# Kernel optimization log

Measured on AMD Instinct MI355X. Metric: run time of the kernel, lower is better.

The kernel has to match this reference:

```python
import jax, jax.numpy as jnp
import numpy as np

LAYERS = 3
EMB = 256
B = 4096
N_ITEMS = 50000
MAX_LEN = 50
EPS = 1e-12  # F.normalize eps


def setup_inputs() -> dict:
    key = jax.random.key(0)
    k1, k2, k3, k4, k5, k6 = jax.random.split(key, 6)
    item_embedding = jax.random.normal(k1, (N_ITEMS, EMB), dtype=jnp.float32)
    D = jax.random.uniform(k2, (B, B), dtype=jnp.float32)
    A = jax.random.uniform(k3, (B, B), dtype=jnp.float32)
    # indices into padded table of size N_ITEMS+1 (row 0 is the zero pad row)
    session_item = jax.random.randint(k4, (B, MAX_LEN), 0, N_ITEMS + 1, dtype=jnp.int64)
    session_len = jax.random.randint(k5, (B, 1), 1, MAX_LEN + 1).astype(jnp.float32)
    w_sess = jax.random.normal(k6, (LAYERS, EMB, EMB), dtype=jnp.float32) * (1.0 / np.sqrt(EMB))
    return {"item_embedding": item_embedding, "D": D, "A": A,
            "session_item": session_item, "session_len": session_len,
            "w_sess": w_sess}


def reference(item_embedding, D, A, session_item, session_len, w_sess):
    # prepend zero pad row, then gather: [B, L, E]
    emb = jnp.concatenate([jnp.zeros((1, item_embedding.shape[1]), item_embedding.dtype),
                           item_embedding], axis=0)
    seq_h = emb[session_item]                      # fused gather (no host round-trip)
    session_emb = seq_h.sum(axis=1) / session_len  # [B, E] mean pooling

    DA = D @ A                                     # [B, B]
    acc = session_emb                              # layer-0 (unnormalized) term
    x = session_emb
    for i in range(LAYERS):
        x = x @ w_sess[i].T                        # torch Linear: y = x W^T
        x = DA @ x                                 # dense GCN propagation
        norm = jnp.maximum(jnp.linalg.norm(x, axis=-1, keepdims=True), EPS)
        acc = acc + x / norm                       # normalized copy stored; x stays raw
    return acc / (LAYERS + 1)
```

## Files before the change

kernel.cpp:

```cpp
#include <hip/hip_runtime.h>
#include <hip/hip_bf16.h>
#include <cstdint>
#include <cstddef>

#define LAYERS 3
#define EMB 256
#define NB 4096
#define MAXLEN 50
#define NITEMS 50000

typedef float f32x4 __attribute__((ext_vector_type(4)));
typedef __bf16 bf16x8 __attribute__((ext_vector_type(8)));
typedef unsigned short u16;

static __device__ __forceinline__ u16 f2bf(float f) {
  union { float f; uint32_t u; } v; v.f = f;
  uint32_t r = v.u + 0x7FFFu + ((v.u >> 16) & 1u);
  return (u16)(r >> 16);
}

static __device__ __forceinline__ float bf2f(u16 h) {
  union { uint32_t u; float f; } v; v.u = (uint32_t)h << 16; return v.f;
}

static __device__ __forceinline__ f32x4 bfu4(ushort4 h) {
  f32x4 r; r.x = bf2f(h.x); r.y = bf2f(h.y); r.z = bf2f(h.z); r.w = bf2f(h.w);
  return r;
}

static __device__ __forceinline__ ushort4 f2bf4(f32x4 v) {
  ushort4 o; o.x = f2bf(v.x); o.y = f2bf(v.y); o.z = f2bf(v.z); o.w = f2bf(v.w);
  return o;
}

template <typename T> __device__ __forceinline__ T cvt_out(float v);
template <> __device__ __forceinline__ float cvt_out<float>(float v) { return v; }
template <> __device__ __forceinline__ u16 cvt_out<u16>(float v) { return f2bf(v); }

#define N4_D (NB * NB / 4)
#define N4_W (LAYERS * EMB * EMB / 4)
#define N4_E ((NITEMS + 1) * EMB / 4)

__global__ void pack_all(const float* __restrict__ D, const float* __restrict__ A,
                         const float* __restrict__ w, const float* __restrict__ emb,
                         u16* __restrict__ Db, u16* __restrict__ Ab,
                         u16* __restrict__ wb, u16* __restrict__ ebp) {
  const int total = N4_D + N4_D + N4_W + N4_E;
  for (int i = blockIdx.x * blockDim.x + threadIdx.x; i < total;
       i += gridDim.x * blockDim.x) {
    int j = i;
    if (j < N4_D) {
      reinterpret_cast<ushort4*>(Db)[j] = f2bf4(reinterpret_cast<const f32x4*>(D)[j]);
    } else if ((j -= N4_D) < N4_D) {
      reinterpret_cast<ushort4*>(Ab)[j] = f2bf4(reinterpret_cast<const f32x4*>(A)[j]);
    } else if ((j -= N4_D) < N4_W) {
      reinterpret_cast<ushort4*>(wb)[j] = f2bf4(reinterpret_cast<const f32x4*>(w)[j]);
    } else {
      j -= N4_W;
      ushort4 o = {0, 0, 0, 0};
      if (j >= EMB / 4) o = f2bf4(reinterpret_cast<const f32x4*>(emb)[j - EMB / 4]);
      reinterpret_cast<ushort4*>(ebp)[j] = o;
    }
  }
}

__global__ void gather_mean(const u16* __restrict__ ebp, const int* __restrict__ items,
                            const float* __restrict__ slen, float* __restrict__ acc,
                            u16* __restrict__ xb) {
  int w = threadIdx.x >> 6, lane = threadIdx.x & 63;
  int b = blockIdx.x * 4 + w;
  f32x4 s = {0.f, 0.f, 0.f, 0.f};
  const int* it = items + (size_t)b * MAXLEN;
  const int le = lane * 4;
#pragma unroll 2
  for (int l = 0; l < MAXLEN; l += 5) {
    int i0 = it[l], i1 = it[l + 1], i2 = it[l + 2], i3 = it[l + 3], i4 = it[l + 4];
    ushort4 v0 = *reinterpret_cast<const ushort4*>(ebp + (size_t)i0 * EMB + le);
    ushort4 v1 = *reinterpret_cast<const ushort4*>(ebp + (size_t)i1 * EMB + le);
    ushort4 v2 = *reinterpret_cast<const ushort4*>(ebp + (size_t)i2 * EMB + le);
    ushort4 v3 = *reinterpret_cast<const ushort4*>(ebp + (size_t)i3 * EMB + le);
    ushort4 v4 = *reinterpret_cast<const ushort4*>(ebp + (size_t)i4 * EMB + le);
    s += bfu4(v0) + bfu4(v1) + bfu4(v2) + bfu4(v3) + bfu4(v4);
  }
  float inv = 1.0f / slen[b];
  s *= inv;
  *reinterpret_cast<f32x4*>(acc + (size_t)b * EMB + le) = s;
  *reinterpret_cast<ushort4*>(xb + (size_t)b * EMB + le) = f2bf4(s);
}

template <typename OUT_T>
__global__ __launch_bounds__(256, 3) void gemm_bt(const u16* __restrict__ Am,
                                                  const u16* __restrict__ Bt,
                                                  OUT_T* __restrict__ C,
                                                  int M, int N, int K, size_t zstride) {
  __shared__ __align__(16) u16 As[128 * 64];
  __shared__ __align__(16) u16 Bs[128 * 64];
  const int tid = threadIdx.x;
  const int lane = tid & 63;
  const int wid = tid >> 6;
  const int wr = wid >> 1, wc = wid & 1;
  const int row0 = blockIdx.y * 128, col0 = blockIdx.x * 128;
  const int kslice = K / (int)gridDim.z;
  const int kb = blockIdx.z * kslice, ke = kb + kslice;
  C += (size_t)blockIdx.z * zstride;

  f32x4 acc[4][4];
#pragma unroll
  for (int m = 0; m < 4; m++)
#pragma unroll
    for (int n = 0; n < 4; n++)
#pragma unroll
      for (int j = 0; j < 4; j++) acc[m][n][j] = 0.0f;

  const int lrow = lane & 15;
  const int lhi = lane >> 4;
  const int sw7 = lane & 7;
  const int cswz = ((lane & 7) ^ (lane >> 3)) * 8;
  const int srow = wid * 8 + (lane >> 3);

  for (int k0 = kb; k0 < ke; k0 += 64) {
#pragma unroll
    for (int i = 0; i < 4; i++) {
      int r = i * 32 + srow;
      __builtin_amdgcn_global_load_lds(
          (__attribute__((address_space(1))) void*)(Am + (size_t)(row0 + r) * K + k0 + cswz),
          (__attribute__((address_space(3))) void*)(As + (size_t)(i * 256 + wid * 64) * 8),
          16, 0, 0);
      __builtin_amdgcn_global_load_lds(
          (__attribute__((address_space(1))) void*)(Bt + (size_t)(col0 + r) * K + k0 + cswz),
          (__attribute__((address_space(3))) void*)(Bs + (size_t)(i * 256 + wid * 64) * 8),
          16, 0, 0);
    }
    __syncthreads();

#pragma unroll
    for (int kk = 0; kk < 2; kk++) {
      const int co = ((kk * 4 + lhi) ^ sw7) * 8;
      bf16x8 af[4], bfv[4];
#pragma unroll
      for (int m = 0; m < 4; m++)
        af[m] = *reinterpret_cast<const bf16x8*>(As + (wr * 64 + m * 16 + lrow) * 64 + co);
#pragma unroll
      for (int n = 0; n < 4; n++)
        bfv[n] = *reinterpret_cast<const bf16x8*>(Bs + (wc * 64 + n * 16 + lrow) * 64 + co);
#pragma unroll
      for (int m = 0; m < 4; m++)
#pragma unroll
        for (int n = 0; n < 4; n++)
          acc[m][n] = __builtin_amdgcn_mfma_f32_16x16x32_bf16(af[m], bfv[n], acc[m][n], 0, 0, 0);
    }
    __syncthreads();
  }

#pragma unroll
  for (int m = 0; m < 4; m++) {
#pragma unroll
    for (int j = 0; j < 4; j++) {
      int r = row0 + wr * 64 + m * 16 + lhi * 4 + j;
      OUT_T* cp = C + (size_t)r * N + col0 + wc * 64 + lrow;
#pragma unroll
      for (int n = 0; n < 4; n++) cp[n * 16] = cvt_out<OUT_T>(acc[m][n][j]);
    }
  }
}

__global__ __launch_bounds__(256) void gemm_bt64(const u16* __restrict__ Am,
                                                 const u16* __restrict__ Bt,
                                                 u16* __restrict__ C,
                                                 int M, int N, int K) {
  __shared__ u16 As[64 * 32];
  __shared__ u16 Bs[64 * 32];
  const int tid = threadIdx.x;
  const int lane = tid & 63;
  const int wid = tid >> 6;
  const int wr = wid >> 1, wc = wid & 1;
  const int row0 = blockIdx.y * 64, col0 = blockIdx.x * 64;

  f32x4 acc[2][2];
#pragma unroll
  for (int m = 0; m < 2; m++)
#pragma unroll
    for (int n = 0; n < 2; n++)
#pragma unroll
      for (int j = 0; j < 4; j++) acc[m][n][j] = 0.0f;

  const int lrow = lane & 15;
  const int lko = (lane >> 4) * 8;

  for (int k0 = 0; k0 < K; k0 += 32) {
    int r = tid >> 2, c = (tid & 3) * 8;
    const u16* gA = Am + (size_t)(row0 + r) * K + k0 + c;
    const u16* gB = Bt + (size_t)(col0 + r) * K + k0 + c;
    __builtin_amdgcn_global_load_lds(
        (__attribute__((address_space(1))) void*)gA,
        (__attribute__((address_space(3))) void*)(As + (size_t)(wid * 64) * 8), 16, 0, 0);
    __builtin_amdgcn_global_load_lds(
        (__attribute__((address_space(1))) void*)gB,
        (__attribute__((address_space(3))) void*)(Bs + (size_t)(wid * 64) * 8), 16, 0, 0);
    __syncthreads();

    bf16x8 af[2], bfv[2];
#pragma unroll
    for (int m = 0; m < 2; m++)
      af[m] = *reinterpret_cast<const bf16x8*>(As + (wr * 32 + m * 16 + lrow) * 32 + lko);
#pragma unroll
    for (int n = 0; n < 2; n++)
      bfv[n] = *reinterpret_cast<const bf16x8*>(Bs + (wc * 32 + n * 16 + lrow) * 32 + lko);
#pragma unroll
    for (int m = 0; m < 2; m++)
#pragma unroll
      for (int n = 0; n < 2; n++)
        acc[m][n] = __builtin_amdgcn_mfma_f32_16x16x32_bf16(af[m], bfv[n], acc[m][n], 0, 0, 0);
    __syncthreads();
  }

#pragma unroll
  for (int m = 0; m < 2; m++) {
#pragma unroll
    for (int j = 0; j < 4; j++) {
      int r = row0 + wr * 32 + m * 16 + (lane >> 4) * 4 + j;
      u16* cp = C + (size_t)r * N + col0 + wc * 32 + (lane & 15);
#pragma unroll
      for (int n = 0; n < 2; n++) cp[n * 16] = f2bf(acc[m][n][j]);
    }
  }
}

__global__ void uredux(const u16* __restrict__ zp, u16* __restrict__ uT,
                       int n4, int nsplit, size_t zstride4) {
  int i = blockIdx.x * blockDim.x + threadIdx.x;
  if (i < n4) {
    f32x4 s = {0.f, 0.f, 0.f, 0.f};
    for (int k = 0; k < nsplit; k++)
      s += bfu4(reinterpret_cast<const ushort4*>(zp)[(size_t)k * zstride4 + i]);
    reinterpret_cast<ushort4*>(uT)[i] = f2bf4(s);
  }
}

__global__ void norm_acc(const u16* __restrict__ zp, size_t zstride, int nsplit,
                         float* __restrict__ acc, u16* __restrict__ xb,
                         float* __restrict__ outp, int fin) {
  int b = blockIdx.x, t = threadIdx.x;
  size_t i = (size_t)b * EMB + t;
  float v = 0.0f;
  for (int s = 0; s < nsplit; s++) v += bf2f(zp[(size_t)s * zstride + i]);
  float s2 = v * v;
#pragma unroll
  for (int o = 32; o > 0; o >>= 1) s2 += __shfl_down(s2, o, 64);
  __shared__ float ws4[4];
  if ((t & 63) == 0) ws4[t >> 6] = s2;
  __syncthreads();
  float tot = ws4[0] + ws4[1] + ws4[2] + ws4[3];
  float rn = 1.0f / fmaxf(sqrtf(tot), 1e-12f);
  if (fin) {
    outp[i] = (acc[i] + v * rn) * 0.25f;
  } else {
    acc[i] += v * rn;
    xb[i] = f2bf(v);
  }
}

extern "C" void kernel_launch(void* const* d_in, const int* in_sizes, int n_in,
                              void* d_out, int out_size, void* d_ws, size_t ws_size,
                              hipStream_t stream) {
  const float* emb   = (const float*)d_in[0];
  const float* D     = (const float*)d_in[1];
  const float* A     = (const float*)d_in[2];
  const int*   items = (const int*)d_in[3];
  const float* slen  = (const float*)d_in[4];
  const float* w     = (const float*)d_in[5];
  float* out = (float*)d_out;

  char* p = (char*)d_ws;
  u16* Db   = (u16*)p;   p += (size_t)NB * NB * 2;
  u16* Ab   = (u16*)p;   p += (size_t)NB * NB * 2;
  float* accf = (float*)p; p += (size_t)NB * EMB * 4;
  u16* xb   = (u16*)p;   p += (size_t)NB * EMB * 2;
  u16* yT   = (u16*)p;   p += (size_t)EMB * NB * 2;
  u16* uT   = (u16*)p;   p += (size_t)EMB * NB * 2;
  u16* wb   = (u16*)p;   p += (size_t)LAYERS * EMB * EMB * 2;
  u16* ebp  = (u16*)p;   p += (size_t)(NITEMS + 1) * EMB * 2;
  u16* zp   = ebp;

  pack_all<<<2048, 256, 0, stream>>>(D, A, w, emb, Db, Ab, wb, ebp);
  gather_mean<<<NB / 4, 256, 0, stream>>>(ebp, items, slen, accf, xb);

  for (int i = 0; i < LAYERS; i++) {
    gemm_bt64<<<dim3(NB / 64, EMB / 64), 256, 0, stream>>>(wb + (size_t)i * EMB * EMB, xb, yT,
                                                           EMB, NB, EMB);
    gemm_bt<u16><<<dim3(NB / 128, EMB / 128, 8), 256, 0, stream>>>(
        yT, Ab, zp, EMB, NB, NB, (size_t)EMB * NB);
    uredux<<<EMB * NB / 4 / 256, 256, 0, stream>>>(zp, uT, EMB * NB / 4, 8,
                                                   (size_t)EMB * NB / 4);
    gemm_bt<u16><<<dim3(EMB / 128, NB / 128, 8), 256, 0, stream>>>(
        Db, uT, zp, NB, EMB, NB, (size_t)NB * EMB);
    norm_acc<<<NB, 256, 0, stream>>>(zp, (size_t)NB * EMB, 8, accf, xb, out, i == LAYERS - 1);
  }
}
```

Before: 214.1 us.

## Drop bf16 pre-packing and feed fp32 D/A/embeddings directly into kernels

Removes the up-front pack kernel that converted D, A and the whole embedding table to bf16. The big split-K GEMMs now stage fp32 tiles of D or A into LDS and convert them to bf16 while loading fragments. The gather reads fp32 embeddings with index-minus-one and masks the pad row. The small weight GEMM now loads its full K=256 tile in one pass instead of looping. The aim is to drop the conversion pass and its large write traffic, at the cost of reading fp32 D and A in every layer, doubling LDS tile size and adding conversion work inside the GEMM inner loop.

```diff
diff --git a/kernel.cpp b/kernel.cpp
--- a/kernel.cpp
+++ b/kernel.cpp
@@ -37,34 +37,12 @@
 template <> __device__ __forceinline__ float cvt_out<float>(float v) { return v; }
 template <> __device__ __forceinline__ u16 cvt_out<u16>(float v) { return f2bf(v); }
 
-#define N4_D (NB * NB / 4)
-#define N4_W (LAYERS * EMB * EMB / 4)
-#define N4_E ((NITEMS + 1) * EMB / 4)
-
-__global__ void pack_all(const float* __restrict__ D, const float* __restrict__ A,
-                         const float* __restrict__ w, const float* __restrict__ emb,
-                         u16* __restrict__ Db, u16* __restrict__ Ab,
-                         u16* __restrict__ wb, u16* __restrict__ ebp) {
-  const int total = N4_D + N4_D + N4_W + N4_E;
-  for (int i = blockIdx.x * blockDim.x + threadIdx.x; i < total;
-       i += gridDim.x * blockDim.x) {
-    int j = i;
-    if (j < N4_D) {
-      reinterpret_cast<ushort4*>(Db)[j] = f2bf4(reinterpret_cast<const f32x4*>(D)[j]);
-    } else if ((j -= N4_D) < N4_D) {
-      reinterpret_cast<ushort4*>(Ab)[j] = f2bf4(reinterpret_cast<const f32x4*>(A)[j]);
-    } else if ((j -= N4_D) < N4_W) {
-      reinterpret_cast<ushort4*>(wb)[j] = f2bf4(reinterpret_cast<const f32x4*>(w)[j]);
-    } else {
-      j -= N4_W;
-      ushort4 o = {0, 0, 0, 0};
-      if (j >= EMB / 4) o = f2bf4(reinterpret_cast<const f32x4*>(emb)[j - EMB / 4]);
-      reinterpret_cast<ushort4*>(ebp)[j] = o;
-    }
-  }
-}
-
-__global__ void gather_mean(const u16* __restrict__ ebp, const int* __restrict__ items,
+__global__ void pack_w(const float* __restrict__ in, u16* __restrict__ out) {
+  int i = blockIdx.x * blockDim.x + threadIdx.x;
+  reinterpret_cast<ushort4*>(out)[i] = f2bf4(reinterpret_cast<const f32x4*>(in)[i]);
+}
+
+__global__ void gather_mean(const float* __restrict__ emb, const int* __restrict__ items,
                             const float* __restrict__ slen, float* __restrict__ acc,
                             u16* __restrict__ xb) {
   int w = threadIdx.x >> 6, lane = threadIdx.x & 63;
@@ -75,12 +53,13 @@
 #pragma unroll 2
   for (int l = 0; l < MAXLEN; l += 5) {
     int i0 = it[l], i1 = it[l + 1], i2 = it[l + 2], i3 = it[l + 3], i4 = it[l + 4];
-    ushort4 v0 = *reinterpret_cast<const ushort4*>(ebp + (size_t)i0 * EMB + le);
-    ushort4 v1 = *reinterpret_cast<const ushort4*>(ebp + (size_t)i1 * EMB + le);
-    ushort4 v2 = *reinterpret_cast<const ushort4*>(ebp + (size_t)i2 * EMB + le);
-    ushort4 v3 = *reinterpret_cast<const ushort4*>(ebp + (size_t)i3 * EMB + le);
-    ushort4 v4 = *reinterpret_cast<const ushort4*>(ebp + (size_t)i4 * EMB + le);
-    s += bfu4(v0) + bfu4(v1) + bfu4(v2) + bfu4(v3) + bfu4(v4);
+    f32x4 v0 = *reinterpret_cast<const f32x4*>(emb + (size_t)(i0 > 0 ? i0 - 1 : 0) * EMB + le);
+    f32x4 v1 = *reinterpret_cast<const f32x4*>(emb + (size_t)(i1 > 0 ? i1 - 1 : 0) * EMB + le);
+    f32x4 v2 = *reinterpret_cast<const f32x4*>(emb + (size_t)(i2 > 0 ? i2 - 1 : 0) * EMB + le);
+    f32x4 v3 = *reinterpret_cast<const f32x4*>(emb + (size_t)(i3 > 0 ? i3 - 1 : 0) * EMB + le);
+    f32x4 v4 = *reinterpret_cast<const f32x4*>(emb + (size_t)(i4 > 0 ? i4 - 1 : 0) * EMB + le);
+    s += v0 * (i0 > 0 ? 1.f : 0.f) + v1 * (i1 > 0 ? 1.f : 0.f) + v2 * (i2 > 0 ? 1.f : 0.f) +
+         v3 * (i3 > 0 ? 1.f : 0.f) + v4 * (i4 > 0 ? 1.f : 0.f);
   }
   float inv = 1.0f / slen[b];
   s *= inv;
@@ -88,13 +67,54 @@
   *reinterpret_cast<ushort4*>(xb + (size_t)b * EMB + le) = f2bf4(s);
 }
 
-template <typename OUT_T>
-__global__ __launch_bounds__(256, 3) void gemm_bt(const u16* __restrict__ Am,
-                                                  const u16* __restrict__ Bt,
+template <bool F32>
+__device__ __forceinline__ void stage_tile(const void* __restrict__ g, char* lds, int rbase,
+                                           int K, int k0, int tid, int wid) {
+  constexpr int CPR = F32 ? 16 : 8;
+  constexpr int NLD = F32 ? 8 : 4;
+#pragma unroll
+  for (int i = 0; i < NLD; i++) {
+    int row = i * (256 / CPR) + (tid / CPR);
+    int sc = (tid % CPR) ^ (row & 7);
+    if constexpr (F32) {
+      const float* src = (const float*)g + (size_t)(rbase + row) * K + k0 + sc * 4;
+      __builtin_amdgcn_global_load_lds(
+          (const __attribute__((address_space(1))) void*)src,
+          (__attribute__((address_space(3))) void*)(lds + (i * 256 + wid * 64) * 16), 16, 0, 0);
+    } else {
+      const u16* src = (const u16*)g + (size_t)(rbase + row) * K + k0 + sc * 8;
+      __builtin_amdgcn_global_load_lds(
+          (const __attribute__((address_space(1))) void*)src,
+          (__attribute__((address_space(3))) void*)(lds + (i * 256 + wid * 64) * 16), 16, 0, 0);
+    }
+  }
+}
+
+template <bool F32>
+__device__ __forceinline__ bf16x8 ld_frag(const char* lds, int row_, int kk, int lhi, int sw7) {
+  if constexpr (F32) {
+    const float* p = (const float*)lds + (size_t)row_ * 64;
+    int cp = kk * 8 + lhi * 2;
+    f32x4 lo = *reinterpret_cast<const f32x4*>(p + ((cp ^ sw7) * 4));
+    f32x4 hi = *reinterpret_cast<const f32x4*>(p + (((cp + 1) ^ sw7) * 4));
+    bf16x8 r;
+    r[0] = (__bf16)lo[0]; r[1] = (__bf16)lo[1]; r[2] = (__bf16)lo[2]; r[3] = (__bf16)lo[3];
+    r[4] = (__bf16)hi[0]; r[5] = (__bf16)hi[1]; r[6] = (__bf16)hi[2]; r[7] = (__bf16)hi[3];
+    return r;
+  } else {
+    const u16* p = (const u16*)lds + (size_t)row_ * 64;
+    int co = ((kk * 4 + lhi) ^ sw7) * 8;
+    return *reinterpret_cast<const bf16x8*>(p + co);
+  }
+}
+
+template <bool AF32, bool BF32, typename OUT_T>
+__global__ __launch_bounds__(256, 3) void gemm_mx(const void* __restrict__ Av,
+                                                  const void* __restrict__ Bv,
                                                   OUT_T* __restrict__ C,
                                                   int M, int N, int K, size_t zstride) {
-  __shared__ __align__(16) u16 As[128 * 64];
-  __shared__ __align__(16) u16 Bs[128 * 64];
+  __shared__ __align__(16) char As[128 * 64 * (AF32 ? 4 : 2)];
+  __shared__ __align__(16) char Bs[128 * 64 * (BF32 ? 4 : 2)];
   const int tid = threadIdx.x;
   const int lane = tid & 63;
   const int wid = tid >> 6;
@@ -115,34 +135,21 @@
   const int lrow = lane & 15;
   const int lhi = lane >> 4;
   const int sw7 = lane & 7;
-  const int cswz = ((lane & 7) ^ (lane >> 3)) * 8;
-  const int srow = wid * 8 + (lane >> 3);
 
   for (int k0 = kb; k0 < ke; k0 += 64) {
-#pragma unroll
-    for (int i = 0; i < 4; i++) {
-      int r = i * 32 + srow;
-      __builtin_amdgcn_global_load_lds(
-          (__attribute__((address_space(1))) void*)(Am + (size_t)(row0 + r) * K + k0 + cswz),
-          (__attribute__((address_space(3))) void*)(As + (size_t)(i * 256 + wid * 64) * 8),
-          16, 0, 0);
-      __builtin_amdgcn_global_load_lds(
-          (__attribute__((address_space(1))) void*)(Bt + (size_t)(col0 + r) * K + k0 + cswz),
-          (__attribute__((address_space(3))) void*)(Bs + (size_t)(i * 256 + wid * 64) * 8),
-          16, 0, 0);
-    }
+    stage_tile<AF32>(Av, As, row0, K, k0, tid, wid);
+    stage_tile<BF32>(Bv, Bs, col0, K, k0, tid, wid);
     __syncthreads();
 
 #pragma unroll
     for (int kk = 0; kk < 2; kk++) {
-      const int co = ((kk * 4 + lhi) ^ sw7) * 8;
       bf16x8 af[4], bfv[4];
 #pragma unroll
       for (int m = 0; m < 4; m++)
-        af[m] = *reinterpret_cast<const bf16x8*>(As + (wr * 64 + m * 16 + lrow) * 64 + co);
+        af[m] = ld_frag<AF32>(As, wr * 64 + m * 16 + lrow, kk, lhi, sw7);
 #pragma unroll
       for (int n = 0; n < 4; n++)
-        bfv[n] = *reinterpret_cast<const bf16x8*>(Bs + (wc * 64 + n * 16 + lrow) * 64 + co);
+        bfv[n] = ld_frag<BF32>(Bs, wc * 64 + n * 16 + lrow, kk, lhi, sw7);
 #pragma unroll
       for (int m = 0; m < 4; m++)
 #pragma unroll
@@ -164,17 +171,32 @@
   }
 }
 
-__global__ __launch_bounds__(256) void gemm_bt64(const u16* __restrict__ Am,
+__global__ __launch_bounds__(256) void gemm64_ss(const u16* __restrict__ Am,
                                                  const u16* __restrict__ Bt,
-                                                 u16* __restrict__ C,
-                                                 int M, int N, int K) {
-  __shared__ u16 As[64 * 32];
-  __shared__ u16 Bs[64 * 32];
+                                                 u16* __restrict__ C, int N) {
+  __shared__ __align__(16) u16 As[64 * 256];
+  __shared__ __align__(16) u16 Bs[64 * 256];
   const int tid = threadIdx.x;
   const int lane = tid & 63;
   const int wid = tid >> 6;
   const int wr = wid >> 1, wc = wid & 1;
   const int row0 = blockIdx.y * 64, col0 = blockIdx.x * 64;
+  const int lrow = lane & 15;
+  const int lhi = lane >> 4;
+  const int sw7 = lane & 7;
+
+#pragma unroll
+  for (int i = 0; i < 8; i++) {
+    int row = i * 8 + (tid >> 5);
+    int sc = (tid & 31) ^ (row & 7);
+    __builtin_amdgcn_global_load_lds(
+        (const __attribute__((address_space(1))) void*)(Am + (size_t)(row0 + row) * EMB + sc * 8),
+        (__attribute__((address_space(3))) void*)((char*)As + (i * 256 + wid * 64) * 16), 16, 0, 0);
+    __builtin_amdgcn_global_load_lds(
+        (const __attribute__((address_space(1))) void*)(Bt + (size_t)(col0 + row) * EMB + sc * 8),
+        (__attribute__((address_space(3))) void*)((char*)Bs + (i * 256 + wid * 64) * 16), 16, 0, 0);
+  }
+  __syncthreads();
 
   f32x4 acc[2][2];
 #pragma unroll
@@ -184,42 +206,29 @@
 #pragma unroll
       for (int j = 0; j < 4; j++) acc[m][n][j] = 0.0f;
 
-  const int lrow = lane & 15;
-  const int lko = (lane >> 4) * 8;
-
-  for (int k0 = 0; k0 < K; k0 += 32) {
-    int r = tid >> 2, c = (tid & 3) * 8;
-    const u16* gA = Am + (size_t)(row0 + r) * K + k0 + c;
-    const u16* gB = Bt + (size_t)(col0 + r) * K + k0 + c;
-    __builtin_amdgcn_global_load_lds(
-        (__attribute__((address_space(1))) void*)gA,
-        (__attribute__((address_space(3))) void*)(As + (size_t)(wid * 64) * 8), 16, 0, 0);
-    __builtin_amdgcn_global_load_lds(
-        (__attribute__((address_space(1))) void*)gB,
-        (__attribute__((address_space(3))) void*)(Bs + (size_t)(wid * 64) * 8), 16, 0, 0);
-    __syncthreads();
-
+#pragma unroll
+  for (int ks = 0; ks < 8; ks++) {
+    const int co = ((ks * 4 + lhi) ^ sw7) * 8;
     bf16x8 af[2], bfv[2];
 #pragma unroll
     for (int m = 0; m < 2; m++)
-      af[m] = *reinterpret_cast<const bf16x8*>(As + (wr * 32 + m * 16 + lrow) * 32 + lko);
+      af[m] = *reinterpret_cast<const bf16x8*>(As + (size_t)(wr * 32 + m * 16 + lrow) * 256 + co);
 #pragma unroll
     for (int n = 0; n < 2; n++)
-      bfv[n] = *reinterpret_cast<const bf16x8*>(Bs + (wc * 32 + n * 16 + lrow) * 32 + lko);
+      bfv[n] = *reinterpret_cast<const bf16x8*>(Bs + (size_t)(wc * 32 + n * 16 + lrow) * 256 + co);
 #pragma unroll
     for (int m = 0; m < 2; m++)
 #pragma unroll
       for (int n = 0; n < 2; n++)
         acc[m][n] = __builtin_amdgcn_mfma_f32_16x16x32_bf16(af[m], bfv[n], acc[m][n], 0, 0, 0);
-    __syncthreads();
   }
 
 #pragma unroll
   for (int m = 0; m < 2; m++) {
 #pragma unroll
     for (int j = 0; j < 4; j++) {
-      int r = row0 + wr * 32 + m * 16 + (lane >> 4) * 4 + j;
-      u16* cp = C + (size_t)r * N + col0 + wc * 32 + (lane & 15);
+      int r = row0 + wr * 32 + m * 16 + lhi * 4 + j;
+      u16* cp = C + (size_t)r * N + col0 + wc * 32 + lrow;
 #pragma unroll
       for (int n = 0; n < 2; n++) cp[n * 16] = f2bf(acc[m][n][j]);
     }
@@ -272,28 +281,25 @@
   float* out = (float*)d_out;
 
   char* p = (char*)d_ws;
-  u16* Db   = (u16*)p;   p += (size_t)NB * NB * 2;
-  u16* Ab   = (u16*)p;   p += (size_t)NB * NB * 2;
+  u16* zp   = (u16*)p;   p += (size_t)8 * NB * EMB * 2;
   float* accf = (float*)p; p += (size_t)NB * EMB * 4;
   u16* xb   = (u16*)p;   p += (size_t)NB * EMB * 2;
   u16* yT   = (u16*)p;   p += (size_t)EMB * NB * 2;
   u16* uT   = (u16*)p;   p += (size_t)EMB * NB * 2;
   u16* wb   = (u16*)p;   p += (size_t)LAYERS * EMB * EMB * 2;
-  u16* ebp  = (u16*)p;   p += (size_t)(NITEMS + 1) * EMB * 2;
-  u16* zp   = ebp;
-
-  pack_all<<<2048, 256, 0, stream>>>(D, A, w, emb, Db, Ab, wb, ebp);
-  gather_mean<<<NB / 4, 256, 0, stream>>>(ebp, items, slen, accf, xb);
+
+  pack_w<<<LAYERS * EMB * EMB / 4 / 256, 256, 0, stream>>>(w, wb);
+  gather_mean<<<NB / 4, 256, 0, stream>>>(emb, items, slen, accf, xb);
 
   for (int i = 0; i < LAYERS; i++) {
-    gemm_bt64<<<dim3(NB / 64, EMB / 64), 256, 0, stream>>>(wb + (size_t)i * EMB * EMB, xb, yT,
-                                                           EMB, NB, EMB);
-    gemm_bt<u16><<<dim3(NB / 128, EMB / 128, 8), 256, 0, stream>>>(
-        yT, Ab, zp, EMB, NB, NB, (size_t)EMB * NB);
+    gemm64_ss<<<dim3(NB / 64, EMB / 64), 256, 0, stream>>>(wb + (size_t)i * EMB * EMB, xb, yT,
+                                                           NB);
+    gemm_mx<false, true, u16><<<dim3(NB / 128, EMB / 128, 8), 256, 0, stream>>>(
+        yT, A, zp, EMB, NB, NB, (size_t)EMB * NB);
     uredux<<<EMB * NB / 4 / 256, 256, 0, stream>>>(zp, uT, EMB * NB / 4, 8,
                                                    (size_t)EMB * NB / 4);
-    gemm_bt<u16><<<dim3(EMB / 128, NB / 128, 8), 256, 0, stream>>>(
-        Db, uT, zp, NB, EMB, NB, (size_t)NB * EMB);
+    gemm_mx<true, false, u16><<<dim3(EMB / 128, NB / 128, 8), 256, 0, stream>>>(
+        D, uT, zp, NB, EMB, NB, (size_t)NB * EMB);
     norm_acc<<<NB, 256, 0, stream>>>(zp, (size_t)NB * EMB, 8, accf, xb, out, i == LAYERS - 1);
   }
 }
```

After: 228.5 us. 1.07x slower.

## Widen big GEMM tiles to 256x128 with 8 waves and stage full-K small GEMM

Applied to the files above, without the earlier changes.

The two large split-K GEMMs now use a templated 512-thread kernel whose tile covers the whole 256-wide EMB dimension. Each A or D tile is therefore loaded once instead of twice, which halves re-reads of the large bf16 operand. The small weight GEMM now loads the full K=256 slab into LDS once with a swizzle, instead of looping over 32-wide K chunks with a barrier each step. The pack kernel also converts 8 elements per thread. The risks are lower occupancy from larger LDS tiles and fewer blocks (256 per large GEMM) to fill the GPU.

```diff
diff --git a/kernel.cpp b/kernel.cpp
--- a/kernel.cpp
+++ b/kernel.cpp
@@ -12,6 +12,7 @@
 typedef float f32x4 __attribute__((ext_vector_type(4)));
 typedef __bf16 bf16x8 __attribute__((ext_vector_type(8)));
 typedef unsigned short u16;
+typedef __attribute__((ext_vector_type(8))) unsigned short u16x8;
 
 static __device__ __forceinline__ u16 f2bf(float f) {
   union { float f; uint32_t u; } v; v.f = f;
@@ -37,30 +38,40 @@
 template <> __device__ __forceinline__ float cvt_out<float>(float v) { return v; }
 template <> __device__ __forceinline__ u16 cvt_out<u16>(float v) { return f2bf(v); }
 
-#define N4_D (NB * NB / 4)
-#define N4_W (LAYERS * EMB * EMB / 4)
-#define N4_E ((NITEMS + 1) * EMB / 4)
+#define N8_D (NB * NB / 8)
+#define N8_W (LAYERS * EMB * EMB / 8)
+#define N8_E ((NITEMS + 1) * EMB / 8)
 
 __global__ void pack_all(const float* __restrict__ D, const float* __restrict__ A,
                          const float* __restrict__ w, const float* __restrict__ emb,
                          u16* __restrict__ Db, u16* __restrict__ Ab,
                          u16* __restrict__ wb, u16* __restrict__ ebp) {
-  const int total = N4_D + N4_D + N4_W + N4_E;
+  const int total = N8_D + N8_D + N8_W + N8_E;
   for (int i = blockIdx.x * blockDim.x + threadIdx.x; i < total;
        i += gridDim.x * blockDim.x) {
     int j = i;
-    if (j < N4_D) {
-      reinterpret_cast<ushort4*>(Db)[j] = f2bf4(reinterpret_cast<const f32x4*>(D)[j]);
-    } else if ((j -= N4_D) < N4_D) {
-      reinterpret_cast<ushort4*>(Ab)[j] = f2bf4(reinterpret_cast<const f32x4*>(A)[j]);
-    } else if ((j -= N4_D) < N4_W) {
-      reinterpret_cast<ushort4*>(wb)[j] = f2bf4(reinterpret_cast<const f32x4*>(w)[j]);
+    const float* src; u16* dst;
+    if (j < N8_D) {
+      src = D + (size_t)j * 8; dst = Db + (size_t)j * 8;
+    } else if ((j -= N8_D) < N8_D) {
+      src = A + (size_t)j * 8; dst = Ab + (size_t)j * 8;
+    } else if ((j -= N8_D) < N8_W) {
+      src = w + (size_t)j * 8; dst = wb + (size_t)j * 8;
     } else {
-      j -= N4_W;
-      ushort4 o = {0, 0, 0, 0};
-      if (j >= EMB / 4) o = f2bf4(reinterpret_cast<const f32x4*>(emb)[j - EMB / 4]);
-      reinterpret_cast<ushort4*>(ebp)[j] = o;
-    }
+      j -= N8_W;
+      dst = ebp + (size_t)j * 8;
+      if (j < EMB / 8) {
+        u16x8 z = {0, 0, 0, 0, 0, 0, 0, 0};
+        *reinterpret_cast<u16x8*>(dst) = z;
+        continue;
+      }
+      src = emb + (size_t)(j - EMB / 8) * 8;
+    }
+    f32x4 lo = *reinterpret_cast<const f32x4*>(src);
+    f32x4 hi = *reinterpret_cast<const f32x4*>(src + 4);
+    ushort4 a = f2bf4(lo), b = f2bf4(hi);
+    u16x8 o = {a.x, a.y, a.z, a.w, b.x, b.y, b.z, b.w};
+    *reinterpret_cast<u16x8*>(dst) = o;
   }
 }
 
@@ -88,18 +99,19 @@
   *reinterpret_cast<ushort4*>(xb + (size_t)b * EMB + le) = f2bf4(s);
 }
 
-template <typename OUT_T>
-__global__ __launch_bounds__(256, 3) void gemm_bt(const u16* __restrict__ Am,
-                                                  const u16* __restrict__ Bt,
-                                                  OUT_T* __restrict__ C,
-                                                  int M, int N, int K, size_t zstride) {
-  __shared__ __align__(16) u16 As[128 * 64];
-  __shared__ __align__(16) u16 Bs[128 * 64];
+template <int WR, int WC, typename OUT_T>
+__global__ __launch_bounds__(512, 4) void gemm_w(const u16* __restrict__ Am,
+                                                 const u16* __restrict__ Bt,
+                                                 OUT_T* __restrict__ C,
+                                                 int M, int N, int K, size_t zstride) {
+  constexpr int TM = WR * 64, TN = WC * 64;
+  __shared__ __align__(16) u16 As[TM * 64];
+  __shared__ __align__(16) u16 Bs[TN * 64];
   const int tid = threadIdx.x;
   const int lane = tid & 63;
   const int wid = tid >> 6;
-  const int wr = wid >> 1, wc = wid & 1;
-  const int row0 = blockIdx.y * 128, col0 = blockIdx.x * 128;
+  const int wm = wid / WC, wn = wid % WC;
+  const int row0 = blockIdx.y * TM, col0 = blockIdx.x * TN;
   const int kslice = K / (int)gridDim.z;
   const int kb = blockIdx.z * kslice, ke = kb + kslice;
   C += (size_t)blockIdx.z * zstride;
@@ -115,21 +127,25 @@
   const int lrow = lane & 15;
   const int lhi = lane >> 4;
   const int sw7 = lane & 7;
-  const int cswz = ((lane & 7) ^ (lane >> 3)) * 8;
-  const int srow = wid * 8 + (lane >> 3);
+  const int srow = tid >> 3;
+  const int schk = tid & 7;
 
   for (int k0 = kb; k0 < ke; k0 += 64) {
 #pragma unroll
-    for (int i = 0; i < 4; i++) {
-      int r = i * 32 + srow;
+    for (int i = 0; i < WR; i++) {
+      int row = i * 64 + srow;
+      int sc = schk ^ (row & 7);
       __builtin_amdgcn_global_load_lds(
-          (__attribute__((address_space(1))) void*)(Am + (size_t)(row0 + r) * K + k0 + cswz),
-          (__attribute__((address_space(3))) void*)(As + (size_t)(i * 256 + wid * 64) * 8),
-          16, 0, 0);
+          (const __attribute__((address_space(1))) void*)(Am + (size_t)(row0 + row) * K + k0 + sc * 8),
+          (__attribute__((address_space(3))) void*)(As + (size_t)(i * 512 + tid) * 8), 16, 0, 0);
+    }
+#pragma unroll
+    for (int i = 0; i < WC; i++) {
+      int row = i * 64 + srow;
+      int sc = schk ^ (row & 7);
       __builtin_amdgcn_global_load_lds(
-          (__attribute__((address_space(1))) void*)(Bt + (size_t)(col0 + r) * K + k0 + cswz),
-          (__attribute__((address_space(3))) void*)(Bs + (size_t)(i * 256 + wid * 64) * 8),
-          16, 0, 0);
+          (const __attribute__((address_space(1))) void*)(Bt + (size_t)(col0 + row) * K + k0 + sc * 8),
+          (__attribute__((address_space(3))) void*)(Bs + (size_t)(i * 512 + tid) * 8), 16, 0, 0);
     }
     __syncthreads();
 
@@ -139,10 +155,10 @@
       bf16x8 af[4], bfv[4];
 #pragma unroll
       for (int m = 0; m < 4; m++)
-        af[m] = *reinterpret_cast<const bf16x8*>(As + (wr * 64 + m * 16 + lrow) * 64 + co);
+        af[m] = *reinterpret_cast<const bf16x8*>(As + (size_t)(wm * 64 + m * 16 + lrow) * 64 + co);
 #pragma unroll
       for (int n = 0; n < 4; n++)
-        bfv[n] = *reinterpret_cast<const bf16x8*>(Bs + (wc * 64 + n * 16 + lrow) * 64 + co);
+        bfv[n] = *reinterpret_cast<const bf16x8*>(Bs + (size_t)(wn * 64 + n * 16 + lrow) * 64 + co);
 #pragma unroll
       for (int m = 0; m < 4; m++)
 #pragma unroll
@@ -156,25 +172,40 @@
   for (int m = 0; m < 4; m++) {
 #pragma unroll
     for (int j = 0; j < 4; j++) {
-      int r = row0 + wr * 64 + m * 16 + lhi * 4 + j;
-      OUT_T* cp = C + (size_t)r * N + col0 + wc * 64 + lrow;
+      int r = row0 + wm * 64 + m * 16 + lhi * 4 + j;
+      OUT_T* cp = C + (size_t)r * N + col0 + wn * 64 + lrow;
 #pragma unroll
       for (int n = 0; n < 4; n++) cp[n * 16] = cvt_out<OUT_T>(acc[m][n][j]);
     }
   }
 }
 
-__global__ __launch_bounds__(256) void gemm_bt64(const u16* __restrict__ Am,
+__global__ __launch_bounds__(256) void gemm64_ss(const u16* __restrict__ Am,
                                                  const u16* __restrict__ Bt,
-                                                 u16* __restrict__ C,
-                                                 int M, int N, int K) {
-  __shared__ u16 As[64 * 32];
-  __shared__ u16 Bs[64 * 32];
+                                                 u16* __restrict__ C, int N) {
+  __shared__ __align__(16) u16 As[64 * 256];
+  __shared__ __align__(16) u16 Bs[64 * 256];
   const int tid = threadIdx.x;
   const int lane = tid & 63;
   const int wid = tid >> 6;
   const int wr = wid >> 1, wc = wid & 1;
   const int row0 = blockIdx.y * 64, col0 = blockIdx.x * 64;
+  const int lrow = lane & 15;
+  const int lhi = lane >> 4;
+  const int sw7 = lane & 7;
+
+#pragma unroll
+  for (int i = 0; i < 8; i++) {
+    int row = i * 8 + (tid >> 5);
+    int sc = (tid & 31) ^ (row & 7);
+    __builtin_amdgcn_global_load_lds(
+        (const __attribute__((address_space(1))) void*)(Am + (size_t)(row0 + row) * EMB + sc * 8),
+        (__attribute__((address_space(3))) void*)((char*)As + (i * 256 + wid * 64) * 16), 16, 0, 0);
+    __builtin_amdgcn_global_load_lds(
+        (const __attribute__((address_space(1))) void*)(Bt + (size_t)(col0 + row) * EMB + sc * 8),
+        (__attribute__((address_space(3))) void*)((char*)Bs + (i * 256 + wid * 64) * 16), 16, 0, 0);
+  }
+  __syncthreads();
 
   f32x4 acc[2][2];
 #pragma unroll
@@ -184,42 +215,29 @@
 #pragma unroll
       for (int j = 0; j < 4; j++) acc[m][n][j] = 0.0f;
 
-  const int lrow = lane & 15;
-  const int lko = (lane >> 4) * 8;
-
-  for (int k0 = 0; k0 < K; k0 += 32) {
-    int r = tid >> 2, c = (tid & 3) * 8;
-    const u16* gA = Am + (size_t)(row0 + r) * K + k0 + c;
-    const u16* gB = Bt + (size_t)(col0 + r) * K + k0 + c;
-    __builtin_amdgcn_global_load_lds(
-        (__attribute__((address_space(1))) void*)gA,
-        (__attribute__((address_space(3))) void*)(As + (size_t)(wid * 64) * 8), 16, 0, 0);
-    __builtin_amdgcn_global_load_lds(
-        (__attribute__((address_space(1))) void*)gB,
-        (__attribute__((address_space(3))) void*)(Bs + (size_t)(wid * 64) * 8), 16, 0, 0);
-    __syncthreads();
-
+#pragma unroll
+  for (int ks = 0; ks < 8; ks++) {
+    const int co = ((ks * 4 + lhi) ^ sw7) * 8;
     bf16x8 af[2], bfv[2];
 #pragma unroll
     for (int m = 0; m < 2; m++)
-      af[m] = *reinterpret_cast<const bf16x8*>(As + (wr * 32 + m * 16 + lrow) * 32 + lko);
+      af[m] = *reinterpret_cast<const bf16x8*>(As + (size_t)(wr * 32 + m * 16 + lrow) * 256 + co);
 #pragma unroll
     for (int n = 0; n < 2; n++)
-      bfv[n] = *reinterpret_cast<const bf16x8*>(Bs + (wc * 32 + n * 16 + lrow) * 32 + lko);
+      bfv[n] = *reinterpret_cast<const bf16x8*>(Bs + (size_t)(wc * 32 + n * 16 + lrow) * 256 + co);
 #pragma unroll
     for (int m = 0; m < 2; m++)
 #pragma unroll
       for (int n = 0; n < 2; n++)
         acc[m][n] = __builtin_amdgcn_mfma_f32_16x16x32_bf16(af[m], bfv[n], acc[m][n], 0, 0, 0);
-    __syncthreads();
   }
 
 #pragma unroll
   for (int m = 0; m < 2; m++) {
 #pragma unroll
     for (int j = 0; j < 4; j++) {
-      int r = row0 + wr * 32 + m * 16 + (lane >> 4) * 4 + j;
-      u16* cp = C + (size_t)r * N + col0 + wc * 32 + (lane & 15);
+      int r = row0 + wr * 32 + m * 16 + lhi * 4 + j;
+      u16* cp = C + (size_t)r * N + col0 + wc * 32 + lrow;
 #pragma unroll
       for (int n = 0; n < 2; n++) cp[n * 16] = f2bf(acc[m][n][j]);
     }
@@ -286,13 +304,13 @@
   gather_mean<<<NB / 4, 256, 0, stream>>>(ebp, items, slen, accf, xb);
 
   for (int i = 0; i < LAYERS; i++) {
-    gemm_bt64<<<dim3(NB / 64, EMB / 64), 256, 0, stream>>>(wb + (size_t)i * EMB * EMB, xb, yT,
-                                                           EMB, NB, EMB);
-    gemm_bt<u16><<<dim3(NB / 128, EMB / 128, 8), 256, 0, stream>>>(
+    gemm64_ss<<<dim3(NB / 64, EMB / 64), 256, 0, stream>>>(wb + (size_t)i * EMB * EMB, xb, yT,
+                                                           NB);
+    gemm_w<4, 2, u16><<<dim3(NB / 128, 1, 8), 512, 0, stream>>>(
         yT, Ab, zp, EMB, NB, NB, (size_t)EMB * NB);
     uredux<<<EMB * NB / 4 / 256, 256, 0, stream>>>(zp, uT, EMB * NB / 4, 8,
                                                    (size_t)EMB * NB / 4);
-    gemm_bt<u16><<<dim3(EMB / 128, NB / 128, 8), 256, 0, stream>>>(
+    gemm_w<2, 4, u16><<<dim3(1, NB / 128, 8), 512, 0, stream>>>(
         Db, uT, zp, NB, EMB, NB, (size_t)NB * EMB);
     norm_acc<<<NB, 256, 0, stream>>>(zp, (size_t)NB * EMB, 8, accf, xb, out, i == LAYERS - 1);
   }
```

Result: slower. 229.7 us (+7.3%).
